# Kernel tuning notes

Measured on AMD Instinct MI355X. Metric: run time of the kernel, lower is better.

The kernel has to match this reference:

```python
import jax, jax.numpy as jnp
import numpy as np

B = 65536      # batch
IN_DIM = 1024  # encoder state dim (hid_dim * n_dir * enc_layers)
M = 64         # latent (hypersphere ambient) dim
K = 64         # max rejection-sampling proposals (first-accept selected)


def setup_inputs() -> dict:
    key = jax.random.key(0)
    k1, k2, k3 = jax.random.split(key, 3)
    x = jax.random.normal(k1, (B, IN_DIM), dtype=jnp.float32)
    W_miu = jax.random.normal(k2, (IN_DIM, M), dtype=jnp.float32) * 0.02
    b_miu = jnp.zeros((M,), dtype=jnp.float32)
    W_kappa = jax.random.normal(k3, (IN_DIM, 1), dtype=jnp.float32) * 0.02
    b_kappa = jnp.zeros((1,), dtype=jnp.float32)
    return {"x": x, "W_miu": W_miu, "b_miu": b_miu, "W_kappa": W_kappa, "b_kappa": b_kappa}


def _vmf_rsample(loc, scale, key):
    # loc: (B, M) unit vectors, scale: (B, 1) kappa. Returns z: (B, M).
    m = loc.shape[-1]
    ke, ku, kv = jax.random.split(key, 3)

    # Ulrich/Davidson rejection-sampling envelope params (elementwise over B)
    c = jnp.sqrt(4.0 * scale ** 2 + (m - 1) ** 2)
    b_true = (-2.0 * scale + c) / (m - 1)
    b_app = (m - 1) / (4.0 * scale)
    s = jnp.clip(scale - 10.0, 0.0, 1.0)
    bb = b_app * s + b_true * (1.0 - s)
    a = (m - 1 + 2.0 * scale + c) / 4.0
    d = 4.0 * a * bb / (1.0 + bb) - (m - 1) * np.log(m - 1)

    # K pre-drawn proposals, first-accept selection (equiv. to the torch while-loop)
    half = (m - 1) / 2.0
    e_ = jax.random.beta(ke, half, half, (K, loc.shape[0], 1)).astype(jnp.float32)
    u = jax.random.uniform(ku, (K, loc.shape[0], 1), dtype=jnp.float32, minval=1e-7, maxval=1.0)
    denom = 1.0 - (1.0 - bb) * e_          # (K, B, 1)
    w_all = (1.0 - (1.0 + bb) * e_) / denom
    t = 2.0 * a * bb / denom
    accept = (m - 1) * jnp.log(t) - t + d > jnp.log(u)
    idx = jnp.argmax(accept, axis=0)       # (B, 1), first accepted proposal
    w = jnp.take_along_axis(w_all, idx[None], axis=0)[0]  # (B, 1)

    # tangent direction: uniform on S^{m-2}
    v = jax.random.normal(kv, (loc.shape[0], m - 1), dtype=jnp.float32)
    v = v / jnp.linalg.norm(v, axis=-1, keepdims=True)

    w_perp = jnp.sqrt(jnp.maximum(1.0 - w ** 2, 1e-10))
    x_dir = jnp.concatenate([w, w_perp * v], axis=-1)  # (B, M)

    # Householder rotation mapping e1 -> loc
    e1 = jnp.zeros((m,), dtype=jnp.float32).at[0].set(1.0)
    uh = e1 - loc
    uh = uh / (jnp.linalg.norm(uh, axis=-1, keepdims=True) + 1e-5)
    z = x_dir - 2.0 * jnp.sum(x_dir * uh, axis=-1, keepdims=True) * uh
    return z


def reference(x, W_miu, b_miu, W_kappa, b_kappa):
    miu = x @ W_miu + b_miu
    miu = miu / jnp.linalg.norm(miu, axis=-1, keepdims=True)      # (B, M) mean direction
    kappa = jax.nn.softplus(x @ W_kappa + b_kappa) + 1.0           # (B, 1) concentration
    z = _vmf_rsample(miu, kappa, jax.random.key(42))
    return z
```

## Files before the change

### kernel.cpp

```cpp
#include <hip/hip_runtime.h>
#include <stdint.h>

#pragma clang fp contract(off)

#define BATCH 65536
#define INDIM 1024
#define MDIM  64
#define GROWS 128
#define GBK   32
#define XS    129

struct K2 { uint32_t a, b; };

__device__ __forceinline__ void tf_round(uint32_t &x0, uint32_t &x1, int r) {
  x0 += x1;
  x1 = (x1 << r) | (x1 >> (32 - r));
  x1 ^= x0;
}

__device__ __forceinline__ K2 tf(K2 k, uint32_t c0, uint32_t c1) {
  uint32_t ks0 = k.a, ks1 = k.b, ks2 = k.a ^ k.b ^ 0x1BD11BDAu;
  uint32_t x0 = c0 + ks0, x1 = c1 + ks1;
  tf_round(x0,x1,13); tf_round(x0,x1,15); tf_round(x0,x1,26); tf_round(x0,x1,6);
  x0 += ks1; x1 += ks2 + 1u;
  tf_round(x0,x1,17); tf_round(x0,x1,29); tf_round(x0,x1,16); tf_round(x0,x1,24);
  x0 += ks2; x1 += ks0 + 2u;
  tf_round(x0,x1,13); tf_round(x0,x1,15); tf_round(x0,x1,26); tf_round(x0,x1,6);
  x0 += ks0; x1 += ks1 + 3u;
  tf_round(x0,x1,17); tf_round(x0,x1,29); tf_round(x0,x1,16); tf_round(x0,x1,24);
  x0 += ks1; x1 += ks2 + 4u;
  tf_round(x0,x1,13); tf_round(x0,x1,15); tf_round(x0,x1,26); tf_round(x0,x1,6);
  x0 += ks2; x1 += ks0 + 5u;
  K2 o; o.a = x0; o.b = x1; return o;
}

__device__ __forceinline__ uint32_t rbits32(K2 k, uint32_t idx) {
  K2 r = tf(k, 0u, idx);
  return r.a ^ r.b;
}

__device__ __forceinline__ float u01f(uint32_t bits) {
  return __uint_as_float((bits >> 9) | 0x3f800000u) - 1.0f;
}

__device__ __forceinline__ float xla_log(float x) { return (float)log((double)x); }
__device__ __forceinline__ float xla_exp(float x) { return (float)exp((double)x); }

__device__ __forceinline__ float xla_log1p(float x) {
  float ax = fabsf(x);
  if (ax < 1e-4f) {
    float t = (-0.5f * x) + 1.0f;
    return t * x;
  }
  return xla_log(x + 1.0f);
}

__device__ __forceinline__ float xla_erfinv(float x) {
  float w = -xla_log1p((-x) * x);
  float p;
  if (w < 5.0f) {
    w = w - 2.5f;
    p = 2.81022636e-08f;
    p = 3.43273939e-07f + p * w;
    p = -3.5233877e-06f + p * w;
    p = -4.39150654e-06f + p * w;
    p = 0.00021858087f + p * w;
    p = -0.00125372503f + p * w;
    p = -0.00417768164f + p * w;
    p = 0.246640727f + p * w;
    p = 1.50140941f + p * w;
  } else {
    w = sqrtf(w) - 3.0f;
    p = -0.000200214257f;
    p = 0.000100950558f + p * w;
    p = 0.00134934322f + p * w;
    p = -0.00367342844f + p * w;
    p = 0.00573950773f + p * w;
    p = -0.0076224613f + p * w;
    p = 0.00943887047f + p * w;
    p = 1.00167406f + p * w;
    p = 2.83297682f + p * w;
  }
  return p * x;
}

__device__ __forceinline__ float jr_normal(K2 key) {
  float u01 = u01f(rbits32(key, 0u));
  float uu = u01 * 2.0f + (-0.99999994f);
  uu = fmaxf(-0.99999994f, uu);
  return 1.41421356f * xla_erfinv(uu);
}

__device__ __forceinline__ float gamma315_log(K2 ekey) {
  const float d = 31.5f - 0.33333334f;
  const float c = 0.33333334f / sqrtf(d);
  K2 key = tf(ekey, 0u, 0u);
  float X = 0.0f, V = 1.0f, U = 2.0f;
  while (true) {
    float x4 = (X * X) * (X * X);
    float sq = 1.0f - 0.0331f * x4;
    bool cont = false;
    if (U >= sq) {
      float lv  = xla_log(V);
      float rhs = X * 0.5f + d * ((1.0f - V) + lv);
      cont = (xla_log(U) >= rhs);
    }
    if (!cont) break;
    K2 kn = tf(key, 0u, 0u);
    K2 kx = tf(key, 0u, 1u);
    K2 kU = tf(key, 0u, 2u);
    key = kn;
    float xn, vv;
    K2 xkey = kx;
    do {
      K2 sub = tf(xkey, 0u, 1u);
      xkey = tf(xkey, 0u, 0u);
      xn = jr_normal(sub);
      vv = 1.0f + xn * c;
    } while (vv <= 0.0f);
    X = xn * xn;
    V = (vv * vv) * vv;
    U = u01f(rbits32(kU, 0u));
  }
  return xla_log(d) + xla_log(V);
}

__device__ __forceinline__ float beta315(K2 ka, K2 kb, uint32_t i) {
  float lga = gamma315_log(tf(ka, 0u, i));
  float lgb = gamma315_log(tf(kb, 0u, i));
  float lm = fmaxf(lga, lgb);
  float ea = xla_exp(lga - lm);
  float eb = xla_exp(lgb - lm);
  return ea / (ea + eb);
}

__launch_bounds__(256)
__global__ void gemm_norm_kernel(const float* __restrict__ x,
                                 const float* __restrict__ Wm,
                                 const float* __restrict__ bm,
                                 const float* __restrict__ Wk,
                                 const float* __restrict__ bk,
                                 float* __restrict__ miu_out,
                                 float* __restrict__ kap_out) {
  __shared__ float xsT[GBK * XS];
  __shared__ float ssq[4][GROWS];
  const int t = threadIdx.x;
  const int l = t & 63;
  const int w = t >> 6;
  const int cw = __builtin_amdgcn_readfirstlane(w) * 16;
  const long row0 = (long)blockIdx.x * GROWS;

  float acc0[16], acc1[16];
#pragma unroll
  for (int c = 0; c < 16; ++c) { acc0[c] = 0.0f; acc1[c] = 0.0f; }
  float acck0 = 0.0f, acck1 = 0.0f;

  const int rs = t >> 3;
  const int qs = t & 7;
  float4 st[4];

#define LOADT(K0)                                                              \
  {                                                                            \
    _Pragma("unroll")                                                          \
    for (int lam = 0; lam < 4; ++lam) {                                        \
      int r = rs + 32 * lam;                                                   \
      st[lam] = *(const float4*)(x + (row0 + r) * (long)INDIM + (K0) + 4 * qs);\
    }                                                                          \
  }

  LOADT(0);
  for (int ks = 0; ks < INDIM / GBK; ++ks) {
    __syncthreads();
#pragma unroll
    for (int lam = 0; lam < 4; ++lam) {
      int r = rs + 32 * lam;
      int kb = 4 * qs;
      xsT[(kb + 0) * XS + r] = st[lam].x;
      xsT[(kb + 1) * XS + r] = st[lam].y;
      xsT[(kb + 2) * XS + r] = st[lam].z;
      xsT[(kb + 3) * XS + r] = st[lam].w;
    }
    __syncthreads();
    if (ks + 1 < INDIM / GBK) LOADT((ks + 1) * GBK);

    const float* wbase = Wm + (long)ks * GBK * MDIM + cw;
    if (w == 3) {
#pragma unroll
      for (int kk = 0; kk < GBK; ++kk) {
        float a0 = xsT[kk * XS + l];
        float a1 = xsT[kk * XS + l + 64];
        const float* wr = wbase + (long)kk * MDIM;
        float4 w0 = *(const float4*)(wr);
        float4 w1 = *(const float4*)(wr + 4);
        float4 w2 = *(const float4*)(wr + 8);
        float4 w3 = *(const float4*)(wr + 12);
        const float wv[16] = {w0.x,w0.y,w0.z,w0.w, w1.x,w1.y,w1.z,w1.w,
                              w2.x,w2.y,w2.z,w2.w, w3.x,w3.y,w3.z,w3.w};
#pragma unroll
        for (int c = 0; c < 16; ++c) {
          acc0[c] = fmaf(a0, wv[c], acc0[c]);
          acc1[c] = fmaf(a1, wv[c], acc1[c]);
        }
        float swk = Wk[ks * GBK + kk];
        acck0 = fmaf(a0, swk, acck0);
        acck1 = fmaf(a1, swk, acck1);
      }
    } else {
#pragma unroll
      for (int kk = 0; kk < GBK; ++kk) {
        float a0 = xsT[kk * XS + l];
        float a1 = xsT[kk * XS + l + 64];
        const float* wr = wbase + (long)kk * MDIM;
        float4 w0 = *(const float4*)(wr);
        float4 w1 = *(const float4*)(wr + 4);
        float4 w2 = *(const float4*)(wr + 8);
        float4 w3 = *(const float4*)(wr + 12);
        const float wv[16] = {w0.x,w0.y,w0.z,w0.w, w1.x,w1.y,w1.z,w1.w,
                              w2.x,w2.y,w2.z,w2.w, w3.x,w3.y,w3.z,w3.w};
#pragma unroll
        for (int c = 0; c < 16; ++c) {
          acc0[c] = fmaf(a0, wv[c], acc0[c]);
          acc1[c] = fmaf(a1, wv[c], acc1[c]);
        }
      }
    }
  }

  const float* bmp = bm + cw;
  float4 b0 = *(const float4*)(bmp);
  float4 b1 = *(const float4*)(bmp + 4);
  float4 b2 = *(const float4*)(bmp + 8);
  float4 b3 = *(const float4*)(bmp + 12);
  const float bv[16] = {b0.x,b0.y,b0.z,b0.w, b1.x,b1.y,b1.z,b1.w,
                        b2.x,b2.y,b2.z,b2.w, b3.x,b3.y,b3.z,b3.w};
  float ss0 = 0.0f, ss1 = 0.0f;
#pragma unroll
  for (int c = 0; c < 16; ++c) {
    acc0[c] = acc0[c] + bv[c]; ss0 += acc0[c] * acc0[c];
    acc1[c] = acc1[c] + bv[c]; ss1 += acc1[c] * acc1[c];
  }
  ssq[w][l] = ss0;
  ssq[w][l + 64] = ss1;
  __syncthreads();
  float tot0 = ssq[0][l] + ssq[1][l] + ssq[2][l] + ssq[3][l];
  float tot1 = ssq[0][l + 64] + ssq[1][l + 64] + ssq[2][l + 64] + ssq[3][l + 64];
  float nrm0 = sqrtf(tot0);
  float nrm1 = sqrtf(tot1);
#pragma unroll
  for (int c = 0; c < 16; ++c) { acc0[c] = acc0[c] / nrm0; acc1[c] = acc1[c] / nrm1; }

  float* o0 = miu_out + (row0 + l) * 64 + cw;
  float* o1 = miu_out + (row0 + l + 64) * 64 + cw;
  *(float4*)(o0 + 0)  = make_float4(acc0[0],  acc0[1],  acc0[2],  acc0[3]);
  *(float4*)(o0 + 4)  = make_float4(acc0[4],  acc0[5],  acc0[6],  acc0[7]);
  *(float4*)(o0 + 8)  = make_float4(acc0[8],  acc0[9],  acc0[10], acc0[11]);
  *(float4*)(o0 + 12) = make_float4(acc0[12], acc0[13], acc0[14], acc0[15]);
  *(float4*)(o1 + 0)  = make_float4(acc1[0],  acc1[1],  acc1[2],  acc1[3]);
  *(float4*)(o1 + 4)  = make_float4(acc1[4],  acc1[5],  acc1[6],  acc1[7]);
  *(float4*)(o1 + 8)  = make_float4(acc1[8],  acc1[9],  acc1[10], acc1[11]);
  *(float4*)(o1 + 12) = make_float4(acc1[12], acc1[13], acc1[14], acc1[15]);

  if (w == 3) {
    float y0 = acck0 + bk[0];
    float y1 = acck1 + bk[0];
    float sp0 = fmaxf(y0, 0.0f) + xla_log1p(xla_exp(-fabsf(y0)));
    float sp1 = fmaxf(y1, 0.0f) + xla_log1p(xla_exp(-fabsf(y1)));
    kap_out[row0 + l] = sp0 + 1.0f;
    kap_out[row0 + l + 64] = sp1 + 1.0f;
  }
#undef LOADT
}

__launch_bounds__(64)
__global__ void vmf_sample_kernel(float* __restrict__ z,
                                  const float* __restrict__ kap) {
  __shared__ float vlds[63 * 65];
  __shared__ float wsel_lds[64];
  __shared__ float scale_lds[64];
  const int tl = threadIdx.x;
  const int b = blockIdx.x * 64 + tl;

  K2 root; root.a = 0u; root.b = 42u;
  const K2 ke  = tf(root, 0u, 0u);
  const K2 ku  = tf(root, 0u, 1u);
  const K2 kv  = tf(root, 0u, 2u);
  const K2 kga = tf(ke, 0u, 0u);
  const K2 kgb = tf(ke, 0u, 1u);

  const float kappa = kap[b];
  const float s2 = kappa * kappa;
  const float cenv = sqrtf(4.0f * s2 + 3969.0f);
  const float b_true = (-2.0f * kappa + cenv) / 63.0f;
  const float b_app = 63.0f / (4.0f * kappa);
  const float sclip = fminf(fmaxf(kappa - 10.0f, 0.0f), 1.0f);
  const float bb = b_app * sclip + b_true * (1.0f - sclip);
  const float aenv = (63.0f + 2.0f * kappa + cenv) / 4.0f;
  const float denv = (4.0f * aenv) * bb / (1.0f + bb) - 261.01748776266656f;

  float w_sel = 0.0f, w_first = 0.0f;
  bool found = false;
#pragma unroll 1
  for (uint32_t k = 0; k < 64u && !found; ++k) {
    uint32_t i = k * 65536u + (uint32_t)b;
    float e = beta315(kga, kgb, i);
    float u01 = u01f(rbits32(ku, i));
    float uu = fmaxf(1e-7f, u01 * (1.0f - 1e-7f) + 1e-7f);
    float den = 1.0f - (1.0f - bb) * e;
    float wk = (1.0f - (1.0f + bb) * e) / den;
    float tt = (2.0f * aenv) * bb / den;
    float lhs = 63.0f * xla_log(tt) - tt + denv;
    if (k == 0u) w_first = wk;
    if (lhs > xla_log(uu)) { w_sel = wk; found = true; }
  }
  if (!found) w_sel = w_first;

  float ssum = 0.0f;
#pragma unroll 3
  for (int j = 0; j < 63; ++j) {
    uint32_t fi = (uint32_t)b * 63u + (uint32_t)j;
    float u01 = u01f(rbits32(kv, fi));
    float uu = u01 * 2.0f + (-0.99999994f);
    uu = fmaxf(-0.99999994f, uu);
    float xn = 1.41421356f * xla_erfinv(uu);
    vlds[j * 65 + tl] = xn;
    ssum += xn * xn;
  }
  float vn = sqrtf(ssum);
  float wperp = sqrtf(fmaxf(1.0f - w_sel * w_sel, 1e-10f));
  wsel_lds[tl] = w_sel;
  scale_lds[tl] = wperp / vn;
  __syncthreads();

  const long rowbase = (long)blockIdx.x * 64;
#pragma unroll 1
  for (int r = 0; r < 64; ++r) {
    float mu = z[(rowbase + r) * 64 + tl];
    float uh = (tl == 0 ? 1.0f : 0.0f) - mu;
    int jj = (tl == 0) ? 0 : (tl - 1);
    float xd = (tl == 0) ? wsel_lds[r] : vlds[jj * 65 + r] * scale_lds[r];
    float s1 = uh * uh;
    float sd = xd * uh;
#pragma unroll
    for (int o = 32; o > 0; o >>= 1) {
      s1 += __shfl_xor(s1, o);
      sd += __shfl_xor(sd, o);
    }
    float unorm = sqrtf(s1) + 1e-5f;
    float sc = 2.0f * (sd / unorm);
    z[(rowbase + r) * 64 + tl] = xd - sc * (uh / unorm);
  }
}

extern "C" void kernel_launch(void* const* d_in, const int* in_sizes, int n_in,
                              void* d_out, int out_size, void* d_ws, size_t ws_size,
                              hipStream_t stream) {
  const float* x  = (const float*)d_in[0];
  const float* Wm = (const float*)d_in[1];
  const float* bm = (const float*)d_in[2];
  const float* Wk = (const float*)d_in[3];
  const float* bk = (const float*)d_in[4];
  float* out = (float*)d_out;
  float* kap = (float*)d_ws;

  hipLaunchKernelGGL(gemm_norm_kernel, dim3(BATCH / GROWS), dim3(256), 0, stream,
                     x, Wm, bm, Wk, bk, out, kap);
  hipLaunchKernelGGL(vmf_sample_kernel, dim3(BATCH / 64), dim3(64), 0, stream,
                     out, kap);
}
```

Measured before the change: 630.0 us.

## Stage weights in LDS and parallelize vMF rejection sampling across lanes

The GEMM kernel now cooperatively loads each W_miu/W_kappa k-tile into shared memory alongside x, double-buffered in registers, so the inner loop no longer reads global memory for weights. The sampling kernel moves to 256 threads: four lanes per batch row evaluate proposals in parallel and pick the first accepted one with a ballot, which shortens the serial rejection loop. The tangent normal draw and the Householder step are redistributed so one wave handles a row at a time with lane-parallel erfinv and shuffle reductions, replacing per-thread serial 63-draw loops and the LDS transpose. This adds more shuffles and some redundant proposal evaluations. Its correctness depends on preserving first-accept ordering.

```diff
diff --git a/kernel.cpp b/kernel.cpp
--- a/kernel.cpp
+++ b/kernel.cpp
@@ -143,6 +143,8 @@
                                  float* __restrict__ miu_out,
                                  float* __restrict__ kap_out) {
   __shared__ float xsT[GBK * XS];
+  __shared__ float wlds[GBK * MDIM];
+  __shared__ float wklds[GBK];
   __shared__ float ssq[4][GROWS];
   const int t = threadIdx.x;
   const int l = t & 63;
@@ -158,6 +160,8 @@
   const int rs = t >> 3;
   const int qs = t & 7;
   float4 st[4];
+  float4 ws0, ws1;
+  float wks;
 
 #define LOADT(K0)                                                              \
   {                                                                            \
@@ -167,8 +171,16 @@
       st[lam] = *(const float4*)(x + (row0 + r) * (long)INDIM + (K0) + 4 * qs);\
     }                                                                          \
   }
+#define LOADW(KS)                                                              \
+  {                                                                            \
+    const float* wp = Wm + (long)(KS) * GBK * MDIM + t * 8;                    \
+    ws0 = *(const float4*)(wp);                                                \
+    ws1 = *(const float4*)(wp + 4);                                            \
+    if (t < GBK) wks = Wk[(KS) * GBK + t];                                     \
+  }
 
   LOADT(0);
+  LOADW(0);
   for (int ks = 0; ks < INDIM / GBK; ++ks) {
     __syncthreads();
 #pragma unroll
@@ -180,16 +192,18 @@
       xsT[(kb + 2) * XS + r] = st[lam].z;
       xsT[(kb + 3) * XS + r] = st[lam].w;
     }
+    *(float4*)(&wlds[t * 8])     = ws0;
+    *(float4*)(&wlds[t * 8 + 4]) = ws1;
+    if (t < GBK) wklds[t] = wks;
     __syncthreads();
-    if (ks + 1 < INDIM / GBK) LOADT((ks + 1) * GBK);
-
-    const float* wbase = Wm + (long)ks * GBK * MDIM + cw;
+    if (ks + 1 < INDIM / GBK) { LOADT((ks + 1) * GBK); LOADW(ks + 1); }
+
     if (w == 3) {
 #pragma unroll
       for (int kk = 0; kk < GBK; ++kk) {
         float a0 = xsT[kk * XS + l];
         float a1 = xsT[kk * XS + l + 64];
-        const float* wr = wbase + (long)kk * MDIM;
+        const float* wr = &wlds[kk * MDIM + cw];
         float4 w0 = *(const float4*)(wr);
         float4 w1 = *(const float4*)(wr + 4);
         float4 w2 = *(const float4*)(wr + 8);
@@ -201,7 +215,7 @@
           acc0[c] = fmaf(a0, wv[c], acc0[c]);
           acc1[c] = fmaf(a1, wv[c], acc1[c]);
         }
-        float swk = Wk[ks * GBK + kk];
+        float swk = wklds[kk];
         acck0 = fmaf(a0, swk, acck0);
         acck1 = fmaf(a1, swk, acck1);
       }
@@ -210,7 +224,7 @@
       for (int kk = 0; kk < GBK; ++kk) {
         float a0 = xsT[kk * XS + l];
         float a1 = xsT[kk * XS + l + 64];
-        const float* wr = wbase + (long)kk * MDIM;
+        const float* wr = &wlds[kk * MDIM + cw];
         float4 w0 = *(const float4*)(wr);
         float4 w1 = *(const float4*)(wr + 4);
         float4 w2 = *(const float4*)(wr + 8);
@@ -269,16 +283,17 @@
     kap_out[row0 + l + 64] = sp1 + 1.0f;
   }
 #undef LOADT
-}
-
-__launch_bounds__(64)
+#undef LOADW
+}
+
+__launch_bounds__(256)
 __global__ void vmf_sample_kernel(float* __restrict__ z,
                                   const float* __restrict__ kap) {
-  __shared__ float vlds[63 * 65];
-  __shared__ float wsel_lds[64];
-  __shared__ float scale_lds[64];
-  const int tl = threadIdx.x;
-  const int b = blockIdx.x * 64 + tl;
+  const int t = threadIdx.x;
+  const int lane = t & 63;
+  const int q = t & 3;
+  const int rowblk = t >> 2;
+  const int gb = blockIdx.x * 64 + rowblk;
 
   K2 root; root.a = 0u; root.b = 42u;
   const K2 ke  = tf(root, 0u, 0u);
@@ -287,7 +302,7 @@
   const K2 kga = tf(ke, 0u, 0u);
   const K2 kgb = tf(ke, 0u, 1u);
 
-  const float kappa = kap[b];
+  const float kappa = kap[gb];
   const float s2 = kappa * kappa;
   const float cenv = sqrtf(4.0f * s2 + 3969.0f);
   const float b_true = (-2.0f * kappa + cenv) / 63.0f;
@@ -300,54 +315,68 @@
   float w_sel = 0.0f, w_first = 0.0f;
   bool found = false;
 #pragma unroll 1
-  for (uint32_t k = 0; k < 64u && !found; ++k) {
-    uint32_t i = k * 65536u + (uint32_t)b;
-    float e = beta315(kga, kgb, i);
-    float u01 = u01f(rbits32(ku, i));
-    float uu = fmaxf(1e-7f, u01 * (1.0f - 1e-7f) + 1e-7f);
-    float den = 1.0f - (1.0f - bb) * e;
-    float wk = (1.0f - (1.0f + bb) * e) / den;
-    float tt = (2.0f * aenv) * bb / den;
-    float lhs = 63.0f * xla_log(tt) - tt + denv;
-    if (k == 0u) w_first = wk;
-    if (lhs > xla_log(uu)) { w_sel = wk; found = true; }
-  }
-  if (!found) w_sel = w_first;
-
-  float ssum = 0.0f;
-#pragma unroll 3
-  for (int j = 0; j < 63; ++j) {
-    uint32_t fi = (uint32_t)b * 63u + (uint32_t)j;
-    float u01 = u01f(rbits32(kv, fi));
-    float uu = u01 * 2.0f + (-0.99999994f);
-    uu = fmaxf(-0.99999994f, uu);
-    float xn = 1.41421356f * xla_erfinv(uu);
-    vlds[j * 65 + tl] = xn;
-    ssum += xn * xn;
-  }
-  float vn = sqrtf(ssum);
-  float wperp = sqrtf(fmaxf(1.0f - w_sel * w_sel, 1e-10f));
-  wsel_lds[tl] = w_sel;
-  scale_lds[tl] = wperp / vn;
-  __syncthreads();
-
-  const long rowbase = (long)blockIdx.x * 64;
+  for (int round = 0; round < 16; ++round) {
+    if (!__any(!found)) break;
+    bool acc = false; float wk = 0.0f;
+    if (!found) {
+      uint32_t k = (uint32_t)(round * 4 + q);
+      uint32_t i = k * 65536u + (uint32_t)gb;
+      float e = beta315(kga, kgb, i);
+      float u01 = u01f(rbits32(ku, i));
+      float uu = fmaxf(1e-7f, u01 * (1.0f - 1e-7f) + 1e-7f);
+      float den = 1.0f - (1.0f - bb) * e;
+      wk = (1.0f - (1.0f + bb) * e) / den;
+      float tt2 = (2.0f * aenv) * bb / den;
+      float lhs = 63.0f * xla_log(tt2) - tt2 + denv;
+      acc = lhs > xla_log(uu);
+      if (round == 0 && q == 0) w_first = wk;
+    }
+    unsigned long long bal = __ballot(acc);
+    unsigned nib = (unsigned)((bal >> ((lane >> 2) << 2)) & 0xFull);
+    int winner = nib ? (__ffs(nib) - 1) : 0;
+    float wcand = __shfl(wk, (lane & 60) + winner);
+    if (!found && nib) { w_sel = wcand; found = true; }
+  }
+  float wf = __shfl(w_first, lane & 60);
+  if (!found) w_sel = wf;
+
+  const int wv = t >> 6;
 #pragma unroll 1
-  for (int r = 0; r < 64; ++r) {
-    float mu = z[(rowbase + r) * 64 + tl];
-    float uh = (tl == 0 ? 1.0f : 0.0f) - mu;
-    int jj = (tl == 0) ? 0 : (tl - 1);
-    float xd = (tl == 0) ? wsel_lds[r] : vlds[jj * 65 + r] * scale_lds[r];
-    float s1 = uh * uh;
-    float sd = xd * uh;
-#pragma unroll
-    for (int o = 32; o > 0; o >>= 1) {
-      s1 += __shfl_xor(s1, o);
-      sd += __shfl_xor(sd, o);
-    }
-    float unorm = sqrtf(s1) + 1e-5f;
-    float sc = 2.0f * (sd / unorm);
-    z[(rowbase + r) * 64 + tl] = xd - sc * (uh / unorm);
+  for (int rr = 0; rr < 16; ++rr) {
+    const int rib = wv * 16 + rr;
+    const long gr = (long)blockIdx.x * 64 + rib;
+    float wsel_r = __shfl(w_sel, rr * 4);
+
+    float xn = 0.0f;
+    if (lane < 63) {
+      uint32_t fi = (uint32_t)gr * 63u + (uint32_t)lane;
+      float u01 = u01f(rbits32(kv, fi));
+      float uu = u01 * 2.0f + (-0.99999994f);
+      uu = fmaxf(-0.99999994f, uu);
+      xn = 1.41421356f * xla_erfinv(uu);
+    }
+    float ss = xn * xn;
+#pragma unroll
+    for (int o = 32; o > 0; o >>= 1) ss += __shfl_xor(ss, o);
+    float vn = sqrtf(ss);
+    float wperp = sqrtf(fmaxf(1.0f - wsel_r * wsel_r, 1e-10f));
+
+    float xs_ = __shfl_up(xn, 1);
+    float xd = (lane == 0) ? wsel_r : wperp * (xs_ / vn);
+
+    float mu = z[gr * 64 + lane];
+    float uh = ((lane == 0) ? 1.0f : 0.0f) - mu;
+    float uss = uh * uh;
+#pragma unroll
+    for (int o = 32; o > 0; o >>= 1) uss += __shfl_xor(uss, o);
+    float unorm = sqrtf(uss) + 1e-5f;
+    float uhn = uh / unorm;
+
+    float dd = xd * uhn;
+#pragma unroll
+    for (int o = 32; o > 0; o >>= 1) dd += __shfl_xor(dd, o);
+
+    z[gr * 64 + lane] = xd - 2.0f * dd * uhn;
   }
 }
 
@@ -364,6 +393,6 @@
 
   hipLaunchKernelGGL(gemm_norm_kernel, dim3(BATCH / GROWS), dim3(256), 0, stream,
                      x, Wm, bm, Wk, bk, out, kap);
-  hipLaunchKernelGGL(vmf_sample_kernel, dim3(BATCH / 64), dim3(64), 0, stream,
+  hipLaunchKernelGGL(vmf_sample_kernel, dim3(BATCH / 64), dim3(256), 0, stream,
                      out, kap);
 }
```

Measured after the change: 514.7 us. -18.3%, faster.
